# Performance work log

Measured on AMD Instinct MI355X. Metric: run time of the kernel, lower is better.

Reference implementation:

```python
import jax, jax.numpy as jnp
import numpy as np

B, C, H, W = 64, 256, 32, 32


def setup_inputs() -> dict:
    key = jax.random.key(0)
    ks = jax.random.split(key, 7)
    x1 = jax.random.normal(ks[0], (B, C, H, W), dtype=jnp.float32)
    x2 = jax.random.normal(ks[1], (B, C, H, W), dtype=jnp.float32)
    # 1x1 Conv2d(C+1 -> C, bias=False): weight squeezed to (C, C+1)
    conv_w = jax.random.normal(ks[2], (C, C + 1), dtype=jnp.float32) * (1.0 / np.sqrt(C + 1))
    # caLayer: Conv1d(2->4, k=1) + ReLU + Conv1d(4->1, k=1) + Softmax(dim=1)
    ca_w1 = jax.random.normal(ks[3], (4, 2), dtype=jnp.float32) * (1.0 / np.sqrt(2))
    ca_b1 = jax.random.normal(ks[4], (4,), dtype=jnp.float32) * 0.1
    ca_w2 = jax.random.normal(ks[5], (1, 4), dtype=jnp.float32) * 0.5
    ca_b2 = jax.random.normal(ks[6], (1,), dtype=jnp.float32) * 0.1
    return {"x1": x1, "x2": x2, "conv_w": conv_w, "ca_w1": ca_w1,
            "ca_b1": ca_b1, "ca_w2": ca_w2, "ca_b2": ca_b2}


def _branch_pool(x, conv_w):
    # x: (B, C, H, W)
    b, c, h, w = x.shape
    center = x[:, :, h // 2, w // 2][:, :, None, None]          # (B, C, 1, 1)
    dot = jnp.sum(x * center, axis=1, keepdims=True) / c        # (B, 1, H, W)
    concatenated = jnp.concatenate([x, dot], axis=1)            # (B, C+1, H, W)
    attn = jax.nn.sigmoid(jnp.einsum('oc,bchw->bohw', conv_w, concatenated))
    norm = attn / (jnp.sum(attn, axis=(2, 3), keepdims=True) + 1e-8)
    return jnp.sum(x * norm, axis=(2, 3))                       # (B, C)


def reference(x1, x2, conv_w, ca_w1, ca_b1, ca_w2, ca_b2):
    pooled = jnp.stack([_branch_pool(x1, conv_w),
                        _branch_pool(x2, conv_w)], axis=1)      # (B, 2, C)
    # caLayer: kernel-size-1 Conv1d == channel-mixing matmul over axis 1
    h1 = jax.nn.relu(jnp.einsum('oi,bic->boc', ca_w1, pooled) + ca_b1[None, :, None])
    h2 = jnp.einsum('oi,bic->boc', ca_w2, h1) + ca_b2[None, :, None]  # (B, 1, C)
    x_weights = jax.nn.softmax(h2, axis=1)                      # softmax over size-1 dim
    y_total = pooled * x_weights                                # broadcast (B,2,C)
    return jnp.sum(y_total, axis=1)                             # (B, C)
```

## Files before the change

### kernel.cpp

```cpp
#include <hip/hip_runtime.h>
#include <hip/hip_bf16.h>
#include <math.h>

typedef __bf16 bf16x8 __attribute__((ext_vector_type(8)));
typedef float  f32x16 __attribute__((ext_vector_type(16)));

#define ACCA_OFF  0
#define ACCX_OFF  32768
#define WLAST_OFF 65536
#define WF_OFF    65792

static __device__ __forceinline__ unsigned pkbf(float a, float b) {
    __hip_bfloat162 h = __float22bfloat162_rn(make_float2(a, b));
    unsigned u; __builtin_memcpy(&u, &h, 4); return u;
}

static __device__ __forceinline__ void barrier_lds() {
    asm volatile("s_waitcnt lgkmcnt(0)\n\ts_barrier" ::: "memory");
}

template<int CTRL, int RM>
static __device__ __forceinline__ float dpp_add(float x) {
    int yi = __builtin_amdgcn_update_dpp(0, __builtin_bit_cast(int, x), CTRL, RM, 0xF, true);
    return x + __builtin_bit_cast(float, yi);
}
static __device__ __forceinline__ float red32(float x) {
    x = dpp_add<0x121, 0xF>(x);
    x = dpp_add<0x122, 0xF>(x);
    x = dpp_add<0x124, 0xF>(x);
    x = dpp_add<0x128, 0xF>(x);
    x = dpp_add<0x142, 0xA>(x);
    return x;
}

__global__ void k_init(const float* __restrict__ conv_w, float* __restrict__ ws) {
    int idx = blockIdx.x * 256 + threadIdx.x;
    int j  = idx & 7;
    int l  = (idx >> 3) & 63;
    int ot = (idx >> 9) & 7;
    int S  = idx >> 12;
    int o  = ot * 32 + (l & 31);
    int k  = S * 16 + (l >> 5) * 8 + j;
    ws[WF_OFF + idx] = conv_w[o * 257 + k];
    if (idx < 256) ws[WLAST_OFF + idx] = conv_w[idx * 257 + 256];
    ws[idx] = 0.0f;
}

__global__ __launch_bounds__(512, 2)
void k_main(const float* __restrict__ x1, const float* __restrict__ x2,
            float* __restrict__ ws) {
    int bx = blockIdx.x;
    int xb = bx >> 1;
    int half = bx & 1;
    const float* xpi = ((xb < 64) ? x1 : x2) + (size_t)(xb & 63) * (256 * 1024);
    float* accA = ws + ACCA_OFF + xb * 256;
    float* accX = ws + ACCX_OFF + xb * 256;

    int tid = threadIdx.x;
    int w = tid >> 6;
    int l = tid & 63;
    int lw = l & 31, q = l >> 5;

    __shared__ __align__(16) unsigned sx[16][64][8];
    __shared__ __align__(16) float scen[256];

    int hwi = tid & 15, kc = tid >> 4;

    const float* xbase = xpi + half * 512 + (size_t)(kc * 2) * 1024 + hwi * 4;
    float4 xv[8];
    #pragma unroll
    for (int s = 0; s < 4; ++s) {
        xv[2 * s]     = *(const float4*)(xbase + (size_t)(64 * s) * 1024);
        xv[2 * s + 1] = *(const float4*)(xbase + (size_t)(64 * s + 1) * 1024);
    }
    float cenv = 0.f;
    if (tid < 256) cenv = xpi[(size_t)tid * 1024 + 528];
    float wl = ws[WLAST_OFF + w * 32 + lw] * (1.0f / 256.0f);
    if (tid < 256) scen[tid] = cenv;
    barrier_lds();

    const float* wf = ws + WF_OFF + (size_t)(w * 512 + l * 8);
    bf16x8 A[16];
    #pragma unroll
    for (int S = 0; S < 16; ++S) {
        float4 w0 = *(const float4*)(wf + (size_t)S * 4096);
        float4 w1 = *(const float4*)(wf + (size_t)S * 4096 + 4);
        const float* cp = scen + S * 16 + q * 8;
        float4 c0 = *(const float4*)(cp);
        float4 c1 = *(const float4*)(cp + 4);
        unsigned pw[4];
        pw[0] = pkbf(fmaf(wl, c0.x, w0.x), fmaf(wl, c0.y, w0.y));
        pw[1] = pkbf(fmaf(wl, c0.z, w0.z), fmaf(wl, c0.w, w0.w));
        pw[2] = pkbf(fmaf(wl, c1.x, w1.x), fmaf(wl, c1.y, w1.y));
        pw[3] = pkbf(fmaf(wl, c1.z, w1.z), fmaf(wl, c1.w, w1.w));
        __builtin_memcpy(&A[S], pw, 16);
    }

    int sig = ((lw >> 4) & 1) << 2;
    const unsigned* b0p = &sx[0][lw][(q * 4) ^ sig];
    const unsigned* b1p = &sx[0][32 + lw][(q * 4) ^ sig];

    float sA[16], sX[16];
    #pragma unroll
    for (int r = 0; r < 16; ++r) { sA[r] = 0.f; sX[r] = 0.f; }

    #pragma unroll 1
    for (int t = 0; t < 8; ++t) {
        if (t) barrier_lds();

        #pragma unroll
        for (int s = 0; s < 4; ++s) {
            float4 e = xv[2 * s], o4 = xv[2 * s + 1];
            int S  = (kc >> 3) + 4 * s;
            int wd = kc & 7;
            float ee[4] = {e.x, e.y, e.z, e.w};
            float oo[4] = {o4.x, o4.y, o4.z, o4.w};
            #pragma unroll
            for (int j = 0; j < 4; ++j) {
                int jj  = (hwi + j) & 3;
                int hwr = hwi * 4 + jj;
                sx[S][hwr][wd ^ (((hwr >> 4) & 1) << 2)] = pkbf(ee[jj], oo[jj]);
            }
        }
        if (t < 7) {
            const float* xn = xbase + (t + 1) * 64;
            #pragma unroll
            for (int s = 0; s < 4; ++s) {
                xv[2 * s]     = *(const float4*)(xn + (size_t)(64 * s) * 1024);
                xv[2 * s + 1] = *(const float4*)(xn + (size_t)(64 * s + 1) * 1024);
            }
        }
        barrier_lds();

        f32x16 acc0, acc1;
        #pragma unroll
        for (int e = 0; e < 16; ++e) { acc0[e] = 0.0f; acc1[e] = 0.0f; }
        #pragma unroll
        for (int S = 0; S < 16; ++S) {
            bf16x8 b0, b1;
            __builtin_memcpy(&b0, b0p + S * 512, 16);
            __builtin_memcpy(&b1, b1p + S * 512, 16);
            acc0 = __builtin_amdgcn_mfma_f32_32x32x16_bf16(A[S], b0, acc0, 0, 0, 0);
            acc1 = __builtin_amdgcn_mfma_f32_32x32x16_bf16(A[S], b1, acc1, 0, 0, 0);
        }

        #pragma unroll
        for (int m = 0; m < 4; ++m) {
            int ob = w * 32 + 8 * m + 4 * q;
            int Si = ob >> 4;
            int Wp = ((ob >> 1) & 7) ^ sig;
            unsigned u0[2], u1[2];
            __builtin_memcpy(u0, &sx[Si][lw][Wp], 8);
            __builtin_memcpy(u1, &sx[Si][32 + lw][Wp], 8);
            #pragma unroll
            for (int d = 0; d < 4; ++d) {
                int r = 4 * m + d;
                float a0s = __builtin_amdgcn_rcpf(1.0f + __expf(-acc0[r]));
                float a1s = __builtin_amdgcn_rcpf(1.0f + __expf(-acc1[r]));
                unsigned wa = (d & 2) ? u0[1] : u0[0];
                unsigned wb = (d & 2) ? u1[1] : u1[0];
                float xv0 = (d & 1) ? __builtin_bit_cast(float, wa & 0xffff0000u)
                                    : __builtin_bit_cast(float, wa << 16);
                float xv1 = (d & 1) ? __builtin_bit_cast(float, wb & 0xffff0000u)
                                    : __builtin_bit_cast(float, wb << 16);
                sA[r] += a0s + a1s;
                sX[r] += a0s * xv0 + a1s * xv1;
            }
        }
    }

    #pragma unroll
    for (int r = 0; r < 16; ++r) {
        int row = (r & 3) + 8 * (r >> 2) + 4 * q;
        int o = w * 32 + row;
        float rA = red32(sA[r]);
        float rX = red32(sX[r]);
        if (lw == 31) {
            atomicAdd(&accA[o], rA);
            atomicAdd(&accX[o], rX);
        }
    }
}

__global__ void k_out(const float* __restrict__ ws, float* __restrict__ out) {
    int idx = blockIdx.x * 256 + threadIdx.x;
    int b = idx >> 8, o = idx & 255;
    float a0 = ws[ACCA_OFF + b * 256 + o];
    float p0 = ws[ACCX_OFF + b * 256 + o];
    float a1 = ws[ACCA_OFF + (64 + b) * 256 + o];
    float p1 = ws[ACCX_OFF + (64 + b) * 256 + o];
    out[idx] = p0 / (a0 + 1e-8f) + p1 / (a1 + 1e-8f);
}

extern "C" void kernel_launch(void* const* d_in, const int* in_sizes, int n_in,
                              void* d_out, int out_size, void* d_ws, size_t ws_size,
                              hipStream_t stream) {
    const float* x1     = (const float*)d_in[0];
    const float* x2     = (const float*)d_in[1];
    const float* conv_w = (const float*)d_in[2];
    float* ws  = (float*)d_ws;
    float* out = (float*)d_out;

    k_init<<<256, 256, 0, stream>>>(conv_w, ws);
    k_main<<<256, 512, 0, stream>>>(x1, x2, ws);
    k_out<<<64, 256, 0, stream>>>(ws, out);
}
```

Baseline: 165.2 us.

## Split each image into quarters and reduce with atomics every step

Each image is now split across four blocks instead of two, launching 512 blocks that each process 32 spatial columns per step with a single MFMA tile. The per-thread sA/sX register accumulators are dropped, and the cross-lane reduction plus global atomicAdd now run inside the time loop. The launch bound is raised to allow 4 blocks per CU. The aim is more parallelism and higher occupancy from lower register pressure, at the cost of roughly an order of magnitude more global atomics and reductions.

```diff
diff --git a/kernel.cpp b/kernel.cpp
--- a/kernel.cpp
+++ b/kernel.cpp
@@ -46,12 +46,12 @@
     ws[idx] = 0.0f;
 }
 
-__global__ __launch_bounds__(512, 2)
+__global__ __launch_bounds__(512, 4)
 void k_main(const float* __restrict__ x1, const float* __restrict__ x2,
             float* __restrict__ ws) {
     int bx = blockIdx.x;
-    int xb = bx >> 1;
-    int half = bx & 1;
+    int xb = bx >> 2;
+    int qr = bx & 3;
     const float* xpi = ((xb < 64) ? x1 : x2) + (size_t)(xb & 63) * (256 * 1024);
     float* accA = ws + ACCA_OFF + xb * 256;
     float* accX = ws + ACCX_OFF + xb * 256;
@@ -61,17 +61,17 @@
     int l = tid & 63;
     int lw = l & 31, q = l >> 5;
 
-    __shared__ __align__(16) unsigned sx[16][64][8];
+    __shared__ __align__(16) unsigned sx[16][32][8];
     __shared__ __align__(16) float scen[256];
 
-    int hwi = tid & 15, kc = tid >> 4;
+    int hwi = tid & 7, kc = tid >> 3;
 
-    const float* xbase = xpi + half * 512 + (size_t)(kc * 2) * 1024 + hwi * 4;
-    float4 xv[8];
+    const float* xst = xpi + qr * 256 + (size_t)(kc * 2) * 1024 + hwi * 4;
+    float4 xv[4];
     #pragma unroll
-    for (int s = 0; s < 4; ++s) {
-        xv[2 * s]     = *(const float4*)(xbase + (size_t)(64 * s) * 1024);
-        xv[2 * s + 1] = *(const float4*)(xbase + (size_t)(64 * s + 1) * 1024);
+    for (int s = 0; s < 2; ++s) {
+        xv[2 * s]     = *(const float4*)(xst + (size_t)(128 * s) * 1024);
+        xv[2 * s + 1] = *(const float4*)(xst + (size_t)(128 * s) * 1024 + 1024);
     }
     float cenv = 0.f;
     if (tid < 256) cenv = xpi[(size_t)tid * 1024 + 528];
@@ -96,22 +96,17 @@
         __builtin_memcpy(&A[S], pw, 16);
     }
 
-    int sig = ((lw >> 4) & 1) << 2;
+    int sig = ((lw >> 2) & 1) << 2;
     const unsigned* b0p = &sx[0][lw][(q * 4) ^ sig];
-    const unsigned* b1p = &sx[0][32 + lw][(q * 4) ^ sig];
-
-    float sA[16], sX[16];
-    #pragma unroll
-    for (int r = 0; r < 16; ++r) { sA[r] = 0.f; sX[r] = 0.f; }
 
     #pragma unroll 1
     for (int t = 0; t < 8; ++t) {
         if (t) barrier_lds();
 
         #pragma unroll
-        for (int s = 0; s < 4; ++s) {
+        for (int s = 0; s < 2; ++s) {
             float4 e = xv[2 * s], o4 = xv[2 * s + 1];
-            int S  = (kc >> 3) + 4 * s;
+            int S  = (kc >> 3) + 8 * s;
             int wd = kc & 7;
             float ee[4] = {e.x, e.y, e.z, e.w};
             float oo[4] = {o4.x, o4.y, o4.z, o4.w};
@@ -119,29 +114,27 @@
             for (int j = 0; j < 4; ++j) {
                 int jj  = (hwi + j) & 3;
                 int hwr = hwi * 4 + jj;
-                sx[S][hwr][wd ^ (((hwr >> 4) & 1) << 2)] = pkbf(ee[jj], oo[jj]);
+                sx[S][hwr][wd ^ (((hwr >> 2) & 1) << 2)] = pkbf(ee[jj], oo[jj]);
             }
         }
         if (t < 7) {
-            const float* xn = xbase + (t + 1) * 64;
+            const float* xn = xst + (t + 1) * 32;
             #pragma unroll
-            for (int s = 0; s < 4; ++s) {
-                xv[2 * s]     = *(const float4*)(xn + (size_t)(64 * s) * 1024);
-                xv[2 * s + 1] = *(const float4*)(xn + (size_t)(64 * s + 1) * 1024);
+            for (int s = 0; s < 2; ++s) {
+                xv[2 * s]     = *(const float4*)(xn + (size_t)(128 * s) * 1024);
+                xv[2 * s + 1] = *(const float4*)(xn + (size_t)(128 * s) * 1024 + 1024);
             }
         }
         barrier_lds();
 
-        f32x16 acc0, acc1;
+        f32x16 acc;
         #pragma unroll
-        for (int e = 0; e < 16; ++e) { acc0[e] = 0.0f; acc1[e] = 0.0f; }
+        for (int e = 0; e < 16; ++e) acc[e] = 0.0f;
         #pragma unroll
         for (int S = 0; S < 16; ++S) {
-            bf16x8 b0, b1;
-            __builtin_memcpy(&b0, b0p + S * 512, 16);
-            __builtin_memcpy(&b1, b1p + S * 512, 16);
-            acc0 = __builtin_amdgcn_mfma_f32_32x32x16_bf16(A[S], b0, acc0, 0, 0, 0);
-            acc1 = __builtin_amdgcn_mfma_f32_32x32x16_bf16(A[S], b1, acc1, 0, 0, 0);
+            bf16x8 b0;
+            __builtin_memcpy(&b0, b0p + S * 256, 16);
+            acc = __builtin_amdgcn_mfma_f32_32x32x16_bf16(A[S], b0, acc, 0, 0, 0);
         }
 
         #pragma unroll
@@ -149,35 +142,23 @@
             int ob = w * 32 + 8 * m + 4 * q;
             int Si = ob >> 4;
             int Wp = ((ob >> 1) & 7) ^ sig;
-            unsigned u0[2], u1[2];
+            unsigned u0[2];
             __builtin_memcpy(u0, &sx[Si][lw][Wp], 8);
-            __builtin_memcpy(u1, &sx[Si][32 + lw][Wp], 8);
             #pragma unroll
             for (int d = 0; d < 4; ++d) {
                 int r = 4 * m + d;
-                float a0s = __builtin_amdgcn_rcpf(1.0f + __expf(-acc0[r]));
-                float a1s = __builtin_amdgcn_rcpf(1.0f + __expf(-acc1[r]));
+                int o = ob + d;
+                float a0s = __builtin_amdgcn_rcpf(1.0f + __expf(-acc[r]));
                 unsigned wa = (d & 2) ? u0[1] : u0[0];
-                unsigned wb = (d & 2) ? u1[1] : u1[0];
                 float xv0 = (d & 1) ? __builtin_bit_cast(float, wa & 0xffff0000u)
                                     : __builtin_bit_cast(float, wa << 16);
-                float xv1 = (d & 1) ? __builtin_bit_cast(float, wb & 0xffff0000u)
-                                    : __builtin_bit_cast(float, wb << 16);
-                sA[r] += a0s + a1s;
-                sX[r] += a0s * xv0 + a1s * xv1;
+                float vA = red32(a0s);
+                float vX = red32(a0s * xv0);
+                if (lw == 31) {
+                    atomicAdd(&accA[o], vA);
+                    atomicAdd(&accX[o], vX);
+                }
             }
-        }
-    }
-
-    #pragma unroll
-    for (int r = 0; r < 16; ++r) {
-        int row = (r & 3) + 8 * (r >> 2) + 4 * q;
-        int o = w * 32 + row;
-        float rA = red32(sA[r]);
-        float rX = red32(sX[r]);
-        if (lw == 31) {
-            atomicAdd(&accA[o], rA);
-            atomicAdd(&accX[o], rX);
         }
     }
 }
@@ -202,6 +183,6 @@
     float* out = (float*)d_out;
 
     k_init<<<256, 256, 0, stream>>>(conv_w, ws);
-    k_main<<<256, 512, 0, stream>>>(x1, x2, ws);
+    k_main<<<512, 512, 0, stream>>>(x1, x2, ws);
     k_out<<<64, 256, 0, stream>>>(ws, out);
 }
```

Result: slower. 193.7 us (+17.2%).
